# Kernel optimization log

Measured on AMD Instinct MI355X. Metric: run time of the kernel, lower is better.

The kernel has to match this reference:

```python
import jax, jax.numpy as jnp
import numpy as np

DIM = 512


def layer_norm(x, w, b, eps=1e-5):
    mu = jnp.mean(x, axis=-1, keepdims=True)
    var = jnp.var(x, axis=-1, keepdims=True)
    return (x - mu) * jax.lax.rsqrt(var + eps) * w + b


def setup_inputs() -> dict:
    key = jax.random.key(0)
    kx, = jax.random.split(key, 1)
    x = jax.random.normal(kx, (8, 2048, DIM), dtype=jnp.float32)
    ln_w = jnp.ones((DIM,), dtype=jnp.float32)
    ln_b = jnp.zeros((DIM,), dtype=jnp.float32)
    q_diag = jnp.ones((DIM,), dtype=jnp.float32)
    k_diag = jnp.ones((DIM,), dtype=jnp.float32)
    v_diag = jnp.ones((DIM,), dtype=jnp.float32)
    return {"x": x, "ln_w": ln_w, "ln_b": ln_b,
            "q_diag": q_diag, "k_diag": k_diag, "v_diag": v_diag}


def reference(x, ln_w, ln_b, q_diag, k_diag, v_diag):
    # x: [B, N, D]
    xn = layer_norm(x, ln_w, ln_b)
    q = xn * q_diag
    k = xn * k_diag
    v = xn * v_diag
    scale = 1.0 / jnp.sqrt(jnp.float32(xn.shape[-1]))
    sim = jnp.einsum('bnd,bmd->bnm', q, k) * scale  # [B, N, N]
    attn = jax.nn.softmax(sim, axis=-1)
    atn_x = jnp.einsum('bnm,bmd->bnd', attn, v)
    # dropout is identity at inference (p=0)
    return xn + atn_x
```

## Files before the change

### kernel.cpp

```cpp
#include <hip/hip_runtime.h>
#include <hip/hip_bf16.h>
#include <stdint.h>
#include <math.h>

typedef __bf16 bf16_t;
typedef bf16_t bf16x8 __attribute__((ext_vector_type(8)));
typedef float f32x4 __attribute__((ext_vector_type(4)));

#define B_DIM 8
#define N_DIM 2048
#define D_DIM 512
#define QK_SCALE 0.04419417382415922f
#define M_SHIFT 4.0f

#define KOFF 0
#define VOFF 65536
#define SMEM_TOTAL 131072

__device__ __forceinline__ bf16_t f2bf(float f) {
    uint32_t u = __builtin_bit_cast(uint32_t, f);
    u += 0x7FFFu + ((u >> 16) & 1u);
    uint16_t h = (uint16_t)(u >> 16);
    return __builtin_bit_cast(bf16_t, h);
}

__global__ __launch_bounds__(256) void ln_prep(
    const float* __restrict__ x, const float* __restrict__ w, const float* __restrict__ bia,
    const float* __restrict__ qd, const float* __restrict__ kd,
    float* __restrict__ xn, bf16_t* __restrict__ qb, bf16_t* __restrict__ kb)
{
    int row  = (int)((blockIdx.x * blockDim.x + threadIdx.x) >> 6);
    int lane = threadIdx.x & 63;
    size_t base = (size_t)row * D_DIM + lane * 8;

    float xv[8];
    {
        float4 a0 = *(const float4*)(x + base);
        float4 a1 = *(const float4*)(x + base + 4);
        xv[0]=a0.x; xv[1]=a0.y; xv[2]=a0.z; xv[3]=a0.w;
        xv[4]=a1.x; xv[5]=a1.y; xv[6]=a1.z; xv[7]=a1.w;
    }
    float s = 0.f, s2 = 0.f;
    #pragma unroll
    for (int j = 0; j < 8; j++) { s += xv[j]; s2 += xv[j]*xv[j]; }
    #pragma unroll
    for (int m = 1; m < 64; m <<= 1) {
        s  += __shfl_xor(s,  m);
        s2 += __shfl_xor(s2, m);
    }
    float mu   = s  * (1.f/512.f);
    float var  = s2 * (1.f/512.f) - mu*mu;
    float rstd = rsqrtf(var + 1e-5f);

    int d = lane * 8;
    float wv[8], bv[8], qv[8], kv[8];
    {
        float4 t;
        t = *(const float4*)(w  + d);     wv[0]=t.x; wv[1]=t.y; wv[2]=t.z; wv[3]=t.w;
        t = *(const float4*)(w  + d + 4); wv[4]=t.x; wv[5]=t.y; wv[6]=t.z; wv[7]=t.w;
        t = *(const float4*)(bia+ d);     bv[0]=t.x; bv[1]=t.y; bv[2]=t.z; bv[3]=t.w;
        t = *(const float4*)(bia+ d + 4); bv[4]=t.x; bv[5]=t.y; bv[6]=t.z; bv[7]=t.w;
        t = *(const float4*)(qd + d);     qv[0]=t.x; qv[1]=t.y; qv[2]=t.z; qv[3]=t.w;
        t = *(const float4*)(qd + d + 4); qv[4]=t.x; qv[5]=t.y; qv[6]=t.z; qv[7]=t.w;
        t = *(const float4*)(kd + d);     kv[0]=t.x; kv[1]=t.y; kv[2]=t.z; kv[3]=t.w;
        t = *(const float4*)(kd + d + 4); kv[4]=t.x; kv[5]=t.y; kv[6]=t.z; kv[7]=t.w;
    }

    float xo[8];
    bf16x8 qo, ko;
    #pragma unroll
    for (int j = 0; j < 8; j++) {
        float v = (xv[j] - mu) * rstd * wv[j] + bv[j];
        xo[j] = v;
        qo[j] = f2bf(v * qv[j] * QK_SCALE);
        ko[j] = f2bf(v * kv[j]);
    }
    {
        float4 o0 = {xo[0],xo[1],xo[2],xo[3]};
        float4 o1 = {xo[4],xo[5],xo[6],xo[7]};
        *(float4*)(xn + base)     = o0;
        *(float4*)(xn + base + 4) = o1;
    }
    *(bf16x8*)(qb + base) = qo;
    *(bf16x8*)(kb + base) = ko;
}

__global__ __launch_bounds__(256) void vT_prep(
    const float* __restrict__ xn, const float* __restrict__ vd, bf16_t* __restrict__ vT)
{
    __shared__ bf16_t tile[64][66];
    int b  = blockIdx.z;
    int n0 = blockIdx.x * 64;
    int d0 = blockIdx.y * 64;
    int t  = threadIdx.x;
    #pragma unroll
    for (int p = 0; p < 16; p++) {
        int idx = t + p*256;
        int nl = idx >> 6, dl = idx & 63;
        float v = xn[((size_t)b*N_DIM + n0 + nl)*D_DIM + d0 + dl] * vd[d0 + dl];
        tile[nl][dl] = f2bf(v);
    }
    __syncthreads();
    #pragma unroll
    for (int p = 0; p < 2; p++) {
        int idx = t + p*256;
        int sfull = idx & 7;
        int dl  = idx >> 3;
        int kb  = sfull >> 2;
        int sp  = sfull & 3;
        int g   = sp ^ ((dl >> 1) & 3);
        bf16x8 o;
        #pragma unroll
        for (int e = 0; e < 4; e++) o[e]   = tile[kb*32 + 4*g + e][dl];
        #pragma unroll
        for (int e = 0; e < 4; e++) o[4+e] = tile[kb*32 + 16 + 4*g + e][dl];
        *(bf16x8*)(vT + ((size_t)(b*D_DIM + d0 + dl))*N_DIM + n0 + kb*32 + sp*8) = o;
    }
}

__global__ __launch_bounds__(512, 2) void attn6(
    const bf16_t* __restrict__ qb, const bf16_t* __restrict__ kb,
    const bf16_t* __restrict__ vT, bf16_t* __restrict__ opart, float* __restrict__ stats)
{
    extern __shared__ char smem[];

    const int bid = blockIdx.x;
    const int xcd = bid & 7, jj = bid >> 3;
    const int grp = xcd + 8*(jj >> 4);
    const int qt  = jj & 15;
    const int b   = grp >> 1;
    const int s   = grp & 1;
    const int q0  = qt * 128;
    const int n0base = s * 1024;

    const int tid  = threadIdx.x;
    const int wid  = tid >> 6;
    const int lane = tid & 63;
    const int g    = lane >> 4;
    const int li   = lane & 15;

    const bf16_t* kb_b = kb + (size_t)b * N_DIM * D_DIM;
    const bf16_t* vT_b = vT + (size_t)b * D_DIM * N_DIM;

    bf16x8 qf[16];
    {
        const bf16_t* qp = qb + ((size_t)(b*N_DIM + q0 + wid*16 + li)) * D_DIM + g*8;
        #pragma unroll
        for (int ks = 0; ks < 16; ks++)
            qf[ks] = *(const bf16x8*)(qp + ks*32);
    }

    f32x4 acc[32];
    const f32x4 zf = {0.f, 0.f, 0.f, 0.f};
    #pragma unroll
    for (int j = 0; j < 32; j++) acc[j] = zf;

    float l_r = 0.f;

    const int Lk = (lane ^ wid) * 8;
    auto stageK = [&](int buf, int t) {
        const int kstart = n0base + t*32;
        char* kdst = smem + KOFF + buf*32768;
        #pragma unroll
        for (int v = 0; v < 4; v++) {
            int row = v*8 + wid;
            const bf16_t* src = kb_b + (size_t)(kstart + row)*D_DIM + Lk;
            __builtin_amdgcn_global_load_lds((const void*)src, (void*)(kdst + row*1024), 16, 0, 0);
        }
    };
    auto stageV = [&](int buf, int t) {
        const int kstart = n0base + t*32;
        char* vdst = smem + VOFF + buf*32768 + wid*4096;
        const int drow = wid*64 + (lane >> 2);
        const bf16_t* src0 = vT_b + (size_t)drow*N_DIM + kstart + (lane & 3)*8;
        #pragma unroll
        for (int v = 0; v < 4; v++) {
            __builtin_amdgcn_global_load_lds((const void*)(src0 + (size_t)(v*16)*N_DIM),
                                             (void*)(vdst + v*1024), 16, 0, 0);
        }
    };

    stageK(0, 0);
    stageV(0, 0);
    asm volatile("s_waitcnt vmcnt(0)" ::: "memory");
    __builtin_amdgcn_s_barrier();

    const int sw  = li & 7;
    const int vsw = (g ^ ((li >> 1) & 3)) << 4;

    #pragma unroll 1
    for (int t = 0; t < 32; ++t) {
        const int buf = t & 1;

        if (t < 31) {
            stageK(buf ^ 1, t + 1);
            stageV(buf ^ 1, t + 1);
        }
        __builtin_amdgcn_sched_barrier(0);

        const char* kr0 = smem + KOFF + buf*32768 + li*1024;
        const char* kr1 = kr0 + 16*1024;
        f32x4 s0 = zf, s1 = zf;
        __builtin_amdgcn_s_setprio(1);
        #pragma unroll
        for (int ks = 0; ks < 16; ks++) {
            int phys = (((ks << 2) + g) ^ sw) << 4;
            bf16x8 k0 = *(const bf16x8*)(kr0 + phys);
            bf16x8 k1 = *(const bf16x8*)(kr1 + phys);
            s0 = __builtin_amdgcn_mfma_f32_16x16x32_bf16(k0, qf[ks], s0, 0, 0, 0);
            s1 = __builtin_amdgcn_mfma_f32_16x16x32_bf16(k1, qf[ks], s1, 0, 0, 0);
        }
        __builtin_amdgcn_s_setprio(0);

        float p0[4], p1[4];
        #pragma unroll
        for (int r = 0; r < 4; r++) {
            p0[r] = __expf(s0[r] - M_SHIFT);
            p1[r] = __expf(s1[r] - M_SHIFT);
        }
        l_r += ((p0[0]+p0[1]) + (p0[2]+p0[3])) + ((p1[0]+p1[1]) + (p1[2]+p1[3]));
        bf16x8 af;
        af[0]=f2bf(p0[0]); af[1]=f2bf(p0[1]); af[2]=f2bf(p0[2]); af[3]=f2bf(p0[3]);
        af[4]=f2bf(p1[0]); af[5]=f2bf(p1[1]); af[6]=f2bf(p1[2]); af[7]=f2bf(p1[3]);

        const char* Vb = smem + VOFF + buf*32768 + li*64 + vsw;
        __builtin_amdgcn_s_setprio(1);
        #pragma unroll
        for (int j = 0; j < 32; j++) {
            bf16x8 bv = *(const bf16x8*)(Vb + j*1024);
            acc[j] = __builtin_amdgcn_mfma_f32_16x16x32_bf16(af, bv, acc[j], 0, 0, 0);
        }
        __builtin_amdgcn_s_setprio(0);

        if (t < 31) {
            asm volatile("s_waitcnt vmcnt(0) lgkmcnt(0)" ::: "memory");
            __builtin_amdgcn_s_barrier();
        }
    }

    l_r += __shfl_xor(l_r, 16);
    l_r += __shfl_xor(l_r, 32);

    bf16_t* op = opart + ((size_t)((s*8 + b)*N_DIM) + q0 + wid*16) * D_DIM;
    #pragma unroll
    for (int j = 0; j < 32; j++)
        #pragma unroll
        for (int r = 0; r < 4; r++)
            op[(size_t)(4*g + r)*D_DIM + j*16 + li] = f2bf(acc[j][r]);

    if (lane < 16) {
        stats[(size_t)(s*8 + b)*N_DIM + q0 + wid*16 + lane] = l_r;
    }
}

__global__ __launch_bounds__(256) void merge2(
    const bf16_t* __restrict__ opart, const float* __restrict__ stats, float* __restrict__ out)
{
    int row  = (int)((blockIdx.x * blockDim.x + threadIdx.x) >> 6);
    int lane = threadIdx.x & 63;
    float l0 = stats[row];
    float l1 = stats[(size_t)16384 + row];
    float rden = 1.f / (l0 + l1);
    size_t base = (size_t)row * D_DIM + lane*8;
    bf16x8 a = *(const bf16x8*)(opart + base);
    bf16x8 c = *(const bf16x8*)(opart + (size_t)16384*D_DIM + base);
    float4 x0 = *(const float4*)(out + base);
    float4 x1 = *(const float4*)(out + base + 4);
    float o[8];
    #pragma unroll
    for (int j = 0; j < 8; j++) o[j] = ((float)a[j] + (float)c[j]) * rden;
    float4 r0 = {x0.x + o[0], x0.y + o[1], x0.z + o[2], x0.w + o[3]};
    float4 r1 = {x1.x + o[4], x1.y + o[5], x1.z + o[6], x1.w + o[7]};
    *(float4*)(out + base)     = r0;
    *(float4*)(out + base + 4) = r1;
}

extern "C" void kernel_launch(void* const* d_in, const int* in_sizes, int n_in,
                              void* d_out, int out_size, void* d_ws, size_t ws_size,
                              hipStream_t stream)
{
    const float* x  = (const float*)d_in[0];
    const float* lw = (const float*)d_in[1];
    const float* lb = (const float*)d_in[2];
    const float* qd = (const float*)d_in[3];
    const float* kd = (const float*)d_in[4];
    const float* vd = (const float*)d_in[5];
    float* out = (float*)d_out;

    const size_t MB = 1024u*1024u;
    char* ws = (char*)d_ws;
    bf16_t* qbuf  = (bf16_t*)(ws);
    bf16_t* kbuf  = (bf16_t*)(ws + 16*MB);
    bf16_t* vTb   = (bf16_t*)(ws + 32*MB);
    bf16_t* opart = (bf16_t*)(ws + 48*MB);
    float*  stats = (float*)(ws + 80*MB);

    hipFuncSetAttribute((const void*)attn6, hipFuncAttributeMaxDynamicSharedMemorySize, SMEM_TOTAL);

    ln_prep<<<4096, 256, 0, stream>>>(x, lw, lb, qd, kd, out, qbuf, kbuf);
    vT_prep<<<dim3(32, 8, 8), 256, 0, stream>>>(out, vd, vTb);
    attn6<<<256, 512, SMEM_TOTAL, stream>>>(qbuf, kbuf, vTb, opart, stats);
    merge2<<<4096, 256, 0, stream>>>(opart, stats, out);
}
```

Before: 129.6 us.

## Fuse LN and V-transpose prep, software-pipeline PV matmul, use exp2

Merges the layer-norm and V-transpose kernels into one kernel that builds the transposed V tile in LDS, so the fp32 normalized activations no longer make a round trip through global memory. The normalized residual is stored in bf16 when enough workspace is available, which halves that traffic at some cost in precision. In the attention loop, the PV MFMA for tile t-1 now runs after the QK MFMA for tile t, using a three-slot V buffer. This lets the softmax exponentials overlap with matrix work. The log2(e) factor is folded into the Q scale so a raw v_exp_f32 can be used, and the LDS allocation grows to 160KB.

After: 128.5 us. About the same (-0.8%).

```diff
diff --git a/kernel.cpp b/kernel.cpp
--- a/kernel.cpp
+++ b/kernel.cpp
@@ -10,12 +10,12 @@
 #define B_DIM 8
 #define N_DIM 2048
 #define D_DIM 512
-#define QK_SCALE 0.04419417382415922f
-#define M_SHIFT 4.0f
+#define QK_SCALE_L2E 0.063758716f
+#define M_SHIFT2 5.7707801635558536f
 
 #define KOFF 0
 #define VOFF 65536
-#define SMEM_TOTAL 131072
+#define SMEM_ATTN 163840
 
 __device__ __forceinline__ bf16_t f2bf(float f) {
     uint32_t u = __builtin_bit_cast(uint32_t, f);
@@ -24,36 +24,30 @@
     return __builtin_bit_cast(bf16_t, h);
 }
 
-__global__ __launch_bounds__(256) void ln_prep(
+__device__ __forceinline__ float fexp2(float x) {
+    float r;
+    asm("v_exp_f32 %0, %1" : "=v"(r) : "v"(x));
+    return r;
+}
+
+__global__ __launch_bounds__(512) void prep_fused(
     const float* __restrict__ x, const float* __restrict__ w, const float* __restrict__ bia,
-    const float* __restrict__ qd, const float* __restrict__ kd,
-    float* __restrict__ xn, bf16_t* __restrict__ qb, bf16_t* __restrict__ kb)
+    const float* __restrict__ qd, const float* __restrict__ kd, const float* __restrict__ vd,
+    bf16_t* __restrict__ xnb, float* __restrict__ xnf,
+    bf16_t* __restrict__ qb, bf16_t* __restrict__ kb, bf16_t* __restrict__ vT)
 {
-    int row  = (int)((blockIdx.x * blockDim.x + threadIdx.x) >> 6);
-    int lane = threadIdx.x & 63;
-    size_t base = (size_t)row * D_DIM + lane * 8;
-
-    float xv[8];
-    {
-        float4 a0 = *(const float4*)(x + base);
-        float4 a1 = *(const float4*)(x + base + 4);
-        xv[0]=a0.x; xv[1]=a0.y; xv[2]=a0.z; xv[3]=a0.w;
-        xv[4]=a1.x; xv[5]=a1.y; xv[6]=a1.z; xv[7]=a1.w;
-    }
-    float s = 0.f, s2 = 0.f;
-    #pragma unroll
-    for (int j = 0; j < 8; j++) { s += xv[j]; s2 += xv[j]*xv[j]; }
-    #pragma unroll
-    for (int m = 1; m < 64; m <<= 1) {
-        s  += __shfl_xor(s,  m);
-        s2 += __shfl_xor(s2, m);
-    }
-    float mu   = s  * (1.f/512.f);
-    float var  = s2 * (1.f/512.f) - mu*mu;
-    float rstd = rsqrtf(var + 1e-5f);
-
-    int d = lane * 8;
-    float wv[8], bv[8], qv[8], kv[8];
+    extern __shared__ char pmem[];
+    bf16_t (*vt)[512] = (bf16_t(*)[512])pmem;
+
+    const int bid = blockIdx.x;
+    const int b  = bid >> 5;
+    const int n0 = (bid & 31) * 64;
+    const int tid  = threadIdx.x;
+    const int wid  = tid >> 6;
+    const int lane = tid & 63;
+    const int d    = lane * 8;
+
+    float wv[8], bv[8], qv[8], kv[8], vv[8];
     {
         float4 t;
         t = *(const float4*)(w  + d);     wv[0]=t.x; wv[1]=t.y; wv[2]=t.z; wv[3]=t.w;
@@ -64,61 +58,79 @@
         t = *(const float4*)(qd + d + 4); qv[4]=t.x; qv[5]=t.y; qv[6]=t.z; qv[7]=t.w;
         t = *(const float4*)(kd + d);     kv[0]=t.x; kv[1]=t.y; kv[2]=t.z; kv[3]=t.w;
         t = *(const float4*)(kd + d + 4); kv[4]=t.x; kv[5]=t.y; kv[6]=t.z; kv[7]=t.w;
-    }
-
-    float xo[8];
-    bf16x8 qo, ko;
-    #pragma unroll
-    for (int j = 0; j < 8; j++) {
-        float v = (xv[j] - mu) * rstd * wv[j] + bv[j];
-        xo[j] = v;
-        qo[j] = f2bf(v * qv[j] * QK_SCALE);
-        ko[j] = f2bf(v * kv[j]);
-    }
+        t = *(const float4*)(vd + d);     vv[0]=t.x; vv[1]=t.y; vv[2]=t.z; vv[3]=t.w;
+        t = *(const float4*)(vd + d + 4); vv[4]=t.x; vv[5]=t.y; vv[6]=t.z; vv[7]=t.w;
+    }
+
+    for (int r = 0; r < 8; r++) {
+        int nl = wid*8 + r;
+        size_t row  = (size_t)b*N_DIM + n0 + nl;
+        size_t base = row*D_DIM + d;
+        float xv[8];
+        {
+            float4 a0 = *(const float4*)(x + base);
+            float4 a1 = *(const float4*)(x + base + 4);
+            xv[0]=a0.x; xv[1]=a0.y; xv[2]=a0.z; xv[3]=a0.w;
+            xv[4]=a1.x; xv[5]=a1.y; xv[6]=a1.z; xv[7]=a1.w;
+        }
+        float s = 0.f, s2 = 0.f;
+        #pragma unroll
+        for (int j = 0; j < 8; j++) { s += xv[j]; s2 += xv[j]*xv[j]; }
+        #pragma unroll
+        for (int m = 1; m < 64; m <<= 1) {
+            s  += __shfl_xor(s,  m);
+            s2 += __shfl_xor(s2, m);
+        }
+        float mu   = s  * (1.f/512.f);
+        float var  = s2 * (1.f/512.f) - mu*mu;
+        float rstd = rsqrtf(var + 1e-5f);
+
+        float xo[8];
+        bf16x8 qo, ko, xb, vb;
+        #pragma unroll
+        for (int j = 0; j < 8; j++) {
+            float v = (xv[j] - mu) * rstd * wv[j] + bv[j];
+            xo[j] = v;
+            xb[j] = f2bf(v);
+            qo[j] = f2bf(v * qv[j] * QK_SCALE_L2E);
+            ko[j] = f2bf(v * kv[j]);
+            vb[j] = f2bf(v * vv[j]);
+        }
+        if (xnb) {
+            *(bf16x8*)(xnb + base) = xb;
+        } else {
+            float4 o0 = {xo[0],xo[1],xo[2],xo[3]};
+            float4 o1 = {xo[4],xo[5],xo[6],xo[7]};
+            *(float4*)(xnf + base)     = o0;
+            *(float4*)(xnf + base + 4) = o1;
+        }
+        *(bf16x8*)(qb + base) = qo;
+        *(bf16x8*)(kb + base) = ko;
+        *(bf16x8*)(&vt[nl][d]) = vb;
+    }
+    __syncthreads();
+
     {
-        float4 o0 = {xo[0],xo[1],xo[2],xo[3]};
-        float4 o1 = {xo[4],xo[5],xo[6],xo[7]};
-        *(float4*)(xn + base)     = o0;
-        *(float4*)(xn + base + 4) = o1;
-    }
-    *(bf16x8*)(qb + base) = qo;
-    *(bf16x8*)(kb + base) = ko;
-}
-
-__global__ __launch_bounds__(256) void vT_prep(
-    const float* __restrict__ xn, const float* __restrict__ vd, bf16_t* __restrict__ vT)
-{
-    __shared__ bf16_t tile[64][66];
-    int b  = blockIdx.z;
-    int n0 = blockIdx.x * 64;
-    int d0 = blockIdx.y * 64;
-    int t  = threadIdx.x;
-    #pragma unroll
-    for (int p = 0; p < 16; p++) {
-        int idx = t + p*256;
-        int nl = idx >> 6, dl = idx & 63;
-        float v = xn[((size_t)b*N_DIM + n0 + nl)*D_DIM + d0 + dl] * vd[d0 + dl];
-        tile[nl][dl] = f2bf(v);
-    }
-    __syncthreads();
-    #pragma unroll
-    for (int p = 0; p < 2; p++) {
-        int idx = t + p*256;
-        int sfull = idx & 7;
-        int dl  = idx >> 3;
-        int kb  = sfull >> 2;
-        int sp  = sfull & 3;
-        int g   = sp ^ ((dl >> 1) & 3);
-        bf16x8 o;
-        #pragma unroll
-        for (int e = 0; e < 4; e++) o[e]   = tile[kb*32 + 4*g + e][dl];
-        #pragma unroll
-        for (int e = 0; e < 4; e++) o[4+e] = tile[kb*32 + 16 + 4*g + e][dl];
-        *(bf16x8*)(vT + ((size_t)(b*D_DIM + d0 + dl))*N_DIM + n0 + kb*32 + sp*8) = o;
-    }
-}
-
-__global__ __launch_bounds__(512, 2) void attn6(
+        const int dd = tid;
+        const int salt = (dd >> 1) & 3;
+        bf16_t* vrow = vT + ((size_t)(b*D_DIM + dd))*N_DIM + n0;
+        #pragma unroll
+        for (int kb2 = 0; kb2 < 2; kb2++) {
+            #pragma unroll
+            for (int sp = 0; sp < 4; sp++) {
+                int gg = sp ^ salt;
+                bf16x8 o;
+                #pragma unroll
+                for (int e = 0; e < 4; e++) o[e]   = vt[kb2*32 + 4*gg + e][dd];
+                #pragma unroll
+                for (int e = 0; e < 4; e++) o[4+e] = vt[kb2*32 + 16 + 4*gg + e][dd];
+                *(bf16x8*)(vrow + kb2*32 + sp*8) = o;
+            }
+        }
+    }
+}
+
+__global__ __launch_bounds__(512, 2) void attn7(
     const bf16_t* __restrict__ qb, const bf16_t* __restrict__ kb,
     const bf16_t* __restrict__ vT, bf16_t* __restrict__ opart, float* __restrict__ stats)
 {
@@ -168,9 +180,9 @@
             __builtin_amdgcn_global_load_lds((const void*)src, (void*)(kdst + row*1024), 16, 0, 0);
         }
     };
-    auto stageV = [&](int buf, int t) {
+    auto stageV = [&](int slot, int t) {
         const int kstart = n0base + t*32;
-        char* vdst = smem + VOFF + buf*32768 + wid*4096;
+        char* vdst = smem + VOFF + slot*32768 + wid*4096;
         const int drow = wid*64 + (lane >> 2);
         const bf16_t* src0 = vT_b + (size_t)drow*N_DIM + kstart + (lane & 3)*8;
         #pragma unroll
@@ -188,17 +200,20 @@
     const int sw  = li & 7;
     const int vsw = (g ^ ((li >> 1) & 3)) << 4;
 
+    int snext = 1, sprev = 2;
+    bf16x8 afp = {};
+
     #pragma unroll 1
     for (int t = 0; t < 32; ++t) {
-        const int buf = t & 1;
+        const int kbuf = t & 1;
 
         if (t < 31) {
-            stageK(buf ^ 1, t + 1);
-            stageV(buf ^ 1, t + 1);
+            stageK(kbuf ^ 1, t + 1);
+            stageV(snext, t + 1);
         }
         __builtin_amdgcn_sched_barrier(0);
 
-        const char* kr0 = smem + KOFF + buf*32768 + li*1024;
+        const char* kr0 = smem + KOFF + kbuf*32768 + li*1024;
         const char* kr1 = kr0 + 16*1024;
         f32x4 s0 = zf, s1 = zf;
         __builtin_amdgcn_s_setprio(1);
@@ -212,25 +227,34 @@
         }
         __builtin_amdgcn_s_setprio(0);
 
-        float p0[4], p1[4];
-        #pragma unroll
-        for (int r = 0; r < 4; r++) {
-            p0[r] = __expf(s0[r] - M_SHIFT);
-            p1[r] = __expf(s1[r] - M_SHIFT);
-        }
-        l_r += ((p0[0]+p0[1]) + (p0[2]+p0[3])) + ((p1[0]+p1[1]) + (p1[2]+p1[3]));
-        bf16x8 af;
-        af[0]=f2bf(p0[0]); af[1]=f2bf(p0[1]); af[2]=f2bf(p0[2]); af[3]=f2bf(p0[3]);
-        af[4]=f2bf(p1[0]); af[5]=f2bf(p1[1]); af[6]=f2bf(p1[2]); af[7]=f2bf(p1[3]);
-
-        const char* Vb = smem + VOFF + buf*32768 + li*64 + vsw;
-        __builtin_amdgcn_s_setprio(1);
-        #pragma unroll
-        for (int j = 0; j < 32; j++) {
-            bf16x8 bv = *(const bf16x8*)(Vb + j*1024);
-            acc[j] = __builtin_amdgcn_mfma_f32_16x16x32_bf16(af, bv, acc[j], 0, 0, 0);
-        }
-        __builtin_amdgcn_s_setprio(0);
+        if (t > 0) {
+            const char* Vb = smem + VOFF + sprev*32768 + li*64 + vsw;
+            __builtin_amdgcn_s_setprio(1);
+            #pragma unroll
+            for (int j = 0; j < 32; j++) {
+                bf16x8 bv = *(const bf16x8*)(Vb + j*1024);
+                acc[j] = __builtin_amdgcn_mfma_f32_16x16x32_bf16(afp, bv, acc[j], 0, 0, 0);
+            }
+            __builtin_amdgcn_s_setprio(0);
+        }
+
+        {
+            bf16x8 af;
+            float la = 0.f, lb2 = 0.f;
+            #pragma unroll
+            for (int r = 0; r < 4; r++) {
+                float e0 = fexp2(s0[r] - M_SHIFT2);
+                float e1 = fexp2(s1[r] - M_SHIFT2);
+                la += e0; lb2 += e1;
+                af[r]   = f2bf(e0);
+                af[4+r] = f2bf(e1);
+            }
+            l_r += la + lb2;
+            afp = af;
+        }
+
+        sprev = (sprev + 1 == 3) ? 0 : sprev + 1;
+        snext = (snext + 1 == 3) ? 0 : snext + 1;
 
         if (t < 31) {
             asm volatile("s_waitcnt vmcnt(0) lgkmcnt(0)" ::: "memory");
@@ -238,6 +262,15 @@
         }
     }
 
+    {
+        const char* Vb = smem + VOFF + sprev*32768 + li*64 + vsw;
+        #pragma unroll
+        for (int j = 0; j < 32; j++) {
+            bf16x8 bv = *(const bf16x8*)(Vb + j*1024);
+            acc[j] = __builtin_amdgcn_mfma_f32_16x16x32_bf16(afp, bv, acc[j], 0, 0, 0);
+        }
+    }
+
     l_r += __shfl_xor(l_r, 16);
     l_r += __shfl_xor(l_r, 32);
 
@@ -253,8 +286,9 @@
     }
 }
 
-__global__ __launch_bounds__(256) void merge2(
-    const bf16_t* __restrict__ opart, const float* __restrict__ stats, float* __restrict__ out)
+__global__ __launch_bounds__(256) void merge3(
+    const bf16_t* __restrict__ opart, const float* __restrict__ stats,
+    const bf16_t* __restrict__ xnb, float* __restrict__ out)
 {
     int row  = (int)((blockIdx.x * blockDim.x + threadIdx.x) >> 6);
     int lane = threadIdx.x & 63;
@@ -264,13 +298,22 @@
     size_t base = (size_t)row * D_DIM + lane*8;
     bf16x8 a = *(const bf16x8*)(opart + base);
     bf16x8 c = *(const bf16x8*)(opart + (size_t)16384*D_DIM + base);
-    float4 x0 = *(const float4*)(out + base);
-    float4 x1 = *(const float4*)(out + base + 4);
+    float xv[8];
+    if (xnb) {
+        bf16x8 xb = *(const bf16x8*)(xnb + base);
+        #pragma unroll
+        for (int j = 0; j < 8; j++) xv[j] = (float)xb[j];
+    } else {
+        float4 x0 = *(const float4*)(out + base);
+        float4 x1 = *(const float4*)(out + base + 4);
+        xv[0]=x0.x; xv[1]=x0.y; xv[2]=x0.z; xv[3]=x0.w;
+        xv[4]=x1.x; xv[5]=x1.y; xv[6]=x1.z; xv[7]=x1.w;
+    }
     float o[8];
     #pragma unroll
-    for (int j = 0; j < 8; j++) o[j] = ((float)a[j] + (float)c[j]) * rden;
-    float4 r0 = {x0.x + o[0], x0.y + o[1], x0.z + o[2], x0.w + o[3]};
-    float4 r1 = {x1.x + o[4], x1.y + o[5], x1.z + o[6], x1.w + o[7]};
+    for (int j = 0; j < 8; j++) o[j] = xv[j] + ((float)a[j] + (float)c[j]) * rden;
+    float4 r0 = {o[0], o[1], o[2], o[3]};
+    float4 r1 = {o[4], o[5], o[6], o[7]};
     *(float4*)(out + base)     = r0;
     *(float4*)(out + base + 4) = r1;
 }
@@ -294,11 +337,12 @@
     bf16_t* vTb   = (bf16_t*)(ws + 32*MB);
     bf16_t* opart = (bf16_t*)(ws + 48*MB);
     float*  stats = (float*)(ws + 80*MB);
-
-    hipFuncSetAttribute((const void*)attn6, hipFuncAttributeMaxDynamicSharedMemorySize, SMEM_TOTAL);
-
-    ln_prep<<<4096, 256, 0, stream>>>(x, lw, lb, qd, kd, out, qbuf, kbuf);
-    vT_prep<<<dim3(32, 8, 8), 256, 0, stream>>>(out, vd, vTb);
-    attn6<<<256, 512, SMEM_TOTAL, stream>>>(qbuf, kbuf, vTb, opart, stats);
-    merge2<<<4096, 256, 0, stream>>>(opart, stats, out);
-}
+    bf16_t* xnb   = (ws_size >= 97*MB) ? (bf16_t*)(ws + 81*MB) : nullptr;
+
+    hipFuncSetAttribute((const void*)prep_fused, hipFuncAttributeMaxDynamicSharedMemorySize, 65536);
+    hipFuncSetAttribute((const void*)attn7, hipFuncAttributeMaxDynamicSharedMemorySize, SMEM_ATTN);
+
+    prep_fused<<<256, 512, 65536, stream>>>(x, lw, lb, qd, kd, vd, xnb, out, qbuf, kbuf, vTb);
+    attn7<<<256, 512, SMEM_ATTN, stream>>>(qbuf, kbuf, vTb, opart, stats);
+    merge3<<<4096, 256, 0, stream>>>(opart, stats, xnb, out);
+}
```
